# Kernel tuning notes

Measured on AMD Instinct MI355X. Metric: run time of the kernel, lower is better.

Reference implementation:

```python
import jax, jax.numpy as jnp
import numpy as np

EMBED_DIM = 1024
NUM_HEADS = 16
HEAD_DIM = EMBED_DIM // NUM_HEADS


def setup_inputs() -> dict:
    key = jax.random.key(0)
    ks = jax.random.split(key, 9)
    B, T, C = 2, 2048, EMBED_DIM
    s = 1.0 / np.sqrt(C)
    return {
        "x": jax.random.normal(ks[0], (B, T, C), dtype=jnp.float32),
        "Wq": jax.random.normal(ks[1], (C, C), dtype=jnp.float32) * s,
        "bq": jnp.zeros((C,), dtype=jnp.float32),
        "Wk": jax.random.normal(ks[2], (C, C), dtype=jnp.float32) * s,
        "bk": jnp.zeros((C,), dtype=jnp.float32),
        "Wv": jax.random.normal(ks[3], (C, C), dtype=jnp.float32) * s,
        "bv": jnp.zeros((C,), dtype=jnp.float32),
        "Wo": jax.random.normal(ks[4], (C, C), dtype=jnp.float32) * s,
        "bo": jnp.zeros((C,), dtype=jnp.float32),
    }


def reference(x, Wq, bq, Wk, bk, Wv, bv, Wo, bo):
    B, T, C = x.shape
    H, D = NUM_HEADS, HEAD_DIM
    # projections (torch Linear: x @ W.T + b; here W stored as [in,out])
    q = (x @ Wq + bq).reshape(B, T, H, D).transpose(0, 2, 1, 3)  # [B,H,T,D]
    k = (x @ Wk + bk).reshape(B, T, H, D).transpose(0, 2, 1, 3)
    v = (x @ Wv + bv).reshape(B, T, H, D).transpose(0, 2, 1, 3)
    scores = jnp.einsum("bhtd,bhsd->bhts", q, k) / jnp.sqrt(jnp.float32(D))
    causal = jnp.tril(jnp.ones((T, T), dtype=bool))  # keep lower triangle
    scores = jnp.where(causal, scores, -jnp.inf)
    weights = jax.nn.softmax(scores, axis=-1)
    attended = jnp.einsum("bhts,bhsd->bhtd", weights, v)
    attended = attended.transpose(0, 2, 1, 3).reshape(B, T, C)
    return attended @ Wo + bo
```

## Files before the change

### kernel.cpp

```cpp
#include <hip/hip_runtime.h>
#include <math.h>


#define BLOCK 256

typedef __attribute__((ext_vector_type(8))) short bf16x8;
typedef __attribute__((ext_vector_type(4))) float f32x4;
typedef __attribute__((ext_vector_type(16))) float f32x16;

__device__ inline short f2bf(float f) {
  union { float f; unsigned u; } c; c.f = f;
  unsigned u = c.u;
  unsigned r = (u + 0x7fffu + ((u >> 16) & 1u)) >> 16;
  return (short)r;
}

#define GLD_LDS16(g, l)                                            \
  __builtin_amdgcn_global_load_lds(                                \
      (const __attribute__((address_space(1))) unsigned int*)(g),  \
      (__attribute__((address_space(3))) unsigned int*)(l), 16, 0, 0)


__global__ void cvt_all_kernel(const float* __restrict__ x,
                               const float* __restrict__ Wq, const float* __restrict__ Wk,
                               const float* __restrict__ Wv, const float* __restrict__ Wo,
                               short* __restrict__ xb,
                               short* __restrict__ Wtqkv, short* __restrict__ Wto) {
  int z = blockIdx.z;
  if (z >= 4) {
    int blk = blockIdx.x + (blockIdx.y << 5) + ((z - 4) << 10);
    int i = (blk * 256 + threadIdx.x) * 8;
    float4 a = *(const float4*)(x + i);
    float4 b = *(const float4*)(x + i + 4);
    alignas(16) short o[8];
    o[0] = f2bf(a.x); o[1] = f2bf(a.y); o[2] = f2bf(a.z); o[3] = f2bf(a.w);
    o[4] = f2bf(b.x); o[5] = f2bf(b.y); o[6] = f2bf(b.z); o[7] = f2bf(b.w);
    *(int4*)(xb + i) = *(int4*)o;
    return;
  }
  __shared__ float tile[32][33];
  const float* W = (z == 0) ? Wq : (z == 1) ? Wk : (z == 2) ? Wv : Wo;
  short* outp = (z == 3) ? Wto : (Wtqkv + (size_t)z * 1024 * 1024);
  int k0 = blockIdx.x * 32, n0 = blockIdx.y * 32;
  int tr = threadIdx.x >> 5, tc = threadIdx.x & 31;
#pragma unroll
  for (int i = 0; i < 4; i++)
    tile[tr + i * 8][tc] = W[(k0 + tr + i * 8) * 1024 + n0 + tc];
  __syncthreads();
#pragma unroll
  for (int i = 0; i < 4; i++)
    outp[(n0 + tr + i * 8) * 1024 + k0 + tc] = f2bf(tile[tc][tr + i * 8]);
}


__global__ __launch_bounds__(BLOCK) void gemm_qkv_kernel(
    const short* __restrict__ A, const short* __restrict__ Wt,
    const float* __restrict__ bq, const float* __restrict__ bk,
    const float* __restrict__ bv,
    short* __restrict__ Qo, short* __restrict__ Ko, short* __restrict__ Vo) {
  const int Kd = 1024;
  const float QSCL = 0.18033688011f;
  int p = blockIdx.x;
  int xcd = p & 7, j = p >> 3;
  int m0 = ((xcd & 3) * 8 + (j & 7)) * 128;
  int n0 = ((xcd >> 2) * 12 + (j >> 3)) * 128;
  int t = threadIdx.x;
  int lane = t & 63, wv = t >> 6;
  int quad = lane >> 4, lc = lane & 15;
  int wy = wv >> 1, wx = wv & 1;
  __shared__ short As[3][128 * 32];
  __shared__ short Bs[3][128 * 32];
  f32x4 acc[4][4] = {};
  int r0 = t >> 2;
  int cs = ((t & 3) ^ ((r0 >> 1) & 3)) * 8;
  const short* Arow0 = A + (size_t)(m0 + r0) * Kd + cs;
  const short* Arow1 = A + (size_t)(m0 + r0 + 64) * Kd + cs;
  const short* Brow0 = Wt + (size_t)(n0 + r0) * Kd + cs;
  const short* Brow1 = Wt + (size_t)(n0 + r0 + 64) * Kd + cs;
#define STAGE_QKV(buf, koff)                           \
  do {                                                 \
    GLD_LDS16(Arow0 + (koff), &As[buf][8 * t]);        \
    GLD_LDS16(Arow1 + (koff), &As[buf][8 * t + 2048]); \
    GLD_LDS16(Brow0 + (koff), &Bs[buf][8 * t]);        \
    GLD_LDS16(Brow1 + (koff), &Bs[buf][8 * t + 2048]); \
  } while (0)
  STAGE_QKV(0, 0);
  asm volatile("" ::: "memory");
  STAGE_QKV(1, 32);
  int xq8 = (quad ^ ((lc >> 1) & 3)) * 8;
  int cur = 0, wr = 2;
  for (int step = 0; step < 32; step++) {
    if (step < 30)
      asm volatile("s_waitcnt vmcnt(4) lgkmcnt(0)" ::: "memory");
    else
      asm volatile("s_waitcnt vmcnt(0) lgkmcnt(0)" ::: "memory");
    __builtin_amdgcn_s_barrier();
    asm volatile("" ::: "memory");
    if (step + 2 < 32) STAGE_QKV(wr, (step + 2) * 32);
    bf16x8 af[4], bf[4];
#pragma unroll
    for (int i = 0; i < 4; i++)
      af[i] = *(const bf16x8*)&As[cur][(wy * 64 + i * 16 + lc) * 32 + xq8];
#pragma unroll
    for (int i = 0; i < 4; i++)
      bf[i] = *(const bf16x8*)&Bs[cur][(wx * 64 + i * 16 + lc) * 32 + xq8];
#pragma unroll
    for (int mi = 0; mi < 4; mi++)
#pragma unroll
      for (int ni = 0; ni < 4; ni++)
        acc[mi][ni] = __builtin_amdgcn_mfma_f32_16x16x32_bf16(af[mi], bf[ni], acc[mi][ni], 0, 0, 0);
    cur = (cur == 2) ? 0 : cur + 1;
    wr = (wr == 2) ? 0 : wr + 1;
  }
#undef STAGE_QKV
#pragma unroll
  for (int mi = 0; mi < 4; mi++) {
    int row = m0 + wy * 64 + mi * 16 + quad * 4;
#pragma unroll
    for (int ni = 0; ni < 4; ni++) {
      int col = n0 + wx * 64 + ni * 16 + lc;
      int which = col >> 10;
      int hd = col & 1023;
      int h = hd >> 6, d = hd & 63;
      float bb = (which == 0) ? bq[hd] : (which == 1) ? bk[hd] : bv[hd];
      if (which == 2) {
        alignas(8) short pk[4];
#pragma unroll
        for (int r = 0; r < 4; r++) pk[r] = f2bf(acc[mi][ni][r] + bb);
        int b = row >> 11, tt = row & 2047;
        *(int2*)&Vo[((size_t)(b * 16 + h) * 64 + d) * 2048 + tt] = *(const int2*)pk;
      } else {
#pragma unroll
        for (int r = 0; r < 4; r++) {
          int rw = row + r;
          int b = rw >> 11, tt = rw & 2047;
          float val = acc[mi][ni][r] + bb;
          if (which == 0) {
            Qo[((size_t)(b * 16 + h) * 2048 + tt) * 64 + d] = f2bf(val * QSCL);
          } else {
            Ko[((size_t)(b * 16 + h) * 2048 + tt) * 64 + d] = f2bf(val);
          }
        }
      }
    }
  }
}


__global__ __launch_bounds__(BLOCK) void gemm_out_kernel(
    const short* __restrict__ A, const short* __restrict__ Wt,
    const float* __restrict__ bias, float* __restrict__ Out) {
  const int Kd = 1024;
  int m0 = blockIdx.x * 64, n0 = blockIdx.y * 128;
  int t = threadIdx.x;
  int lane = t & 63, wv = t >> 6;
  int quad = lane >> 4, lc = lane & 15;
  int wy = wv >> 1, wx = wv & 1;
  __shared__ short As[2][64 * 32];
  __shared__ short Bs[2][128 * 32];
  int r0 = t >> 2, c0 = (t & 3) * 8;
  f32x4 acc[2][4] = {};
  const short* Arow0 = A + (size_t)(m0 + r0) * Kd + c0;
  const short* Brow0 = Wt + (size_t)(n0 + r0) * Kd + c0;
  const short* Brow1 = Wt + (size_t)(n0 + r0 + 64) * Kd + c0;
  GLD_LDS16(Arow0, &As[0][8 * t]);
  GLD_LDS16(Brow0, &Bs[0][8 * t]);
  GLD_LDS16(Brow1, &Bs[0][8 * t + 2048]);
  int cur = 0;
  for (int k0 = 0; k0 < Kd; k0 += 32) {
    __syncthreads();
    if (k0 + 32 < Kd) {
      int nxt = cur ^ 1;
      GLD_LDS16(Arow0 + k0 + 32, &As[nxt][8 * t]);
      GLD_LDS16(Brow0 + k0 + 32, &Bs[nxt][8 * t]);
      GLD_LDS16(Brow1 + k0 + 32, &Bs[nxt][8 * t + 2048]);
    }
    bf16x8 af[2], bf[4];
#pragma unroll
    for (int i = 0; i < 2; i++)
      af[i] = *(const bf16x8*)&As[cur][(wy * 32 + i * 16 + lc) * 32 + quad * 8];
#pragma unroll
    for (int i = 0; i < 4; i++)
      bf[i] = *(const bf16x8*)&Bs[cur][(wx * 64 + i * 16 + lc) * 32 + quad * 8];
#pragma unroll
    for (int mi = 0; mi < 2; mi++)
#pragma unroll
      for (int ni = 0; ni < 4; ni++)
        acc[mi][ni] = __builtin_amdgcn_mfma_f32_16x16x32_bf16(af[mi], bf[ni], acc[mi][ni], 0, 0, 0);
    cur ^= 1;
  }
#pragma unroll
  for (int mi = 0; mi < 2; mi++) {
    int row = m0 + wy * 32 + mi * 16 + quad * 4;
#pragma unroll
    for (int ni = 0; ni < 4; ni++) {
      int col = n0 + wx * 64 + ni * 16 + lc;
      float bb = bias[col];
#pragma unroll
      for (int r = 0; r < 4; r++)
        Out[(size_t)(row + r) * 1024 + col] = acc[mi][ni][r] + bb;
    }
  }
}


__global__ __launch_bounds__(BLOCK, 2) void attn_kernel(
    const short* __restrict__ Q, const short* __restrict__ K,
    const short* __restrict__ Vt, short* __restrict__ Oa) {
  int p = blockIdx.x;
  int bh = ((p & 7) << 2) | ((p >> 3) & 3);
  int pair = p >> 5;
  int t = threadIdx.x;
  int lane = t & 63, w = t >> 6;
  int qh = w & 1, kh = w >> 1;
  int ln = lane & 31, lh = lane >> 5;
  const short* Qb = Q + (size_t)bh * 2048 * 64;
  const short* Kb = K + (size_t)bh * 2048 * 64;
  const short* Vg = Vt + (size_t)bh * 64 * 2048;
  int b = bh >> 4, h = bh & 15;

  __shared__ short Kt[2][64 * 64];
  __shared__ short Vs[2][64 * 64];
  __shared__ __align__(16) short Ps[4][32 * 72];
  __shared__ float lx[2][64];
  short* Pw = Ps[w];

  int srow = t >> 3;
  int sw = t & 7;
  const float M2 = 14.5f;
  int xk = ln & 7;

  for (int sp = 0; sp < 2; sp++) {
    int s = sp ? (31 - pair) : pair;
    int q0 = s * 64;
    int q0w = q0 + qh * 32;
    int qmaxw = q0w + 31;
    int ntiles = s + 1;

    bf16x8 qf[4];
#pragma unroll
    for (int c = 0; c < 4; c++)
      qf[c] = *(const bf16x8*)&Qb[(size_t)(q0w + ln) * 64 + c * 16 + lh * 8];

    f32x16 O0 = {}, O1 = {};
    float lsum = 0.f;

#pragma unroll
    for (int i = 0; i < 2; i++) {
      int r = i * 32 + srow;
      int cg = sw ^ (r & 7);
      GLD_LDS16(&Kb[(size_t)r * 64 + cg * 8], &Kt[0][i * 2048 + 8 * t]);
      GLD_LDS16(&Vg[(size_t)r * 2048 + cg * 8], &Vs[0][i * 2048 + 8 * t]);
    }
    int cur = 0;
    for (int kt = 0; kt < ntiles; kt++) {
      __syncthreads();
      if (kt + 1 < ntiles) {
        int kb2 = (kt + 1) * 64;
        int nxt = cur ^ 1;
#pragma unroll
        for (int i = 0; i < 2; i++) {
          int r = i * 32 + srow;
          int cg = sw ^ (r & 7);
          GLD_LDS16(&Kb[(size_t)(kb2 + r) * 64 + cg * 8], &Kt[nxt][i * 2048 + 8 * t]);
          GLD_LDS16(&Vg[(size_t)r * 2048 + kb2 + cg * 8], &Vs[nxt][i * 2048 + 8 * t]);
        }
      }
      int grpbase = kt * 64 + kh * 32;
      if (grpbase <= qmaxw) {
        f32x16 S = {};
#pragma unroll
        for (int c = 0; c < 4; c++) {
          int ch = c * 2 + lh;
          bf16x8 kf = *(const bf16x8*)&Kt[cur][(kh * 32 + ln) * 64 + (ch ^ xk) * 8];
          S = __builtin_amdgcn_mfma_f32_32x32x16_bf16(kf, qf[c], S, 0, 0, 0);
        }
        if (kt == ntiles - 1) {
          int qg = q0w + ln;
#pragma unroll
          for (int reg = 0; reg < 16; reg++) {
            int key = grpbase + (reg & 3) + 8 * (reg >> 2) + 4 * lh;
            if (key > qg) S[reg] = -3.0e38f;
          }
        }
#pragma unroll
        for (int g = 0; g < 4; g++) {
          unsigned u[4];
#pragma unroll
          for (int i = 0; i < 4; i++) {
            union { float f; unsigned v; } cc;
            cc.f = __builtin_amdgcn_exp2f(S[g * 4 + i] - M2);
            lsum += cc.f;
            u[i] = cc.v + 0x8000u;
          }
          int2 pk;
          pk.x = (int)__builtin_amdgcn_perm(u[1], u[0], 0x07060302);
          pk.y = (int)__builtin_amdgcn_perm(u[3], u[2], 0x07060302);
          *(int2*)&Pw[ln * 72 + g * 8 + lh * 4] = pk;
        }
#pragma unroll
        for (int c2 = 0; c2 < 2; c2++) {
          bf16x8 pf = *(const bf16x8*)&Pw[ln * 72 + c2 * 16 + lh * 8];
          int ch = kh * 4 + c2 * 2 + lh;
          bf16x8 v0 = *(const bf16x8*)&Vs[cur][ln * 64 + (ch ^ xk) * 8];
          bf16x8 v1 = *(const bf16x8*)&Vs[cur][(32 + ln) * 64 + (ch ^ xk) * 8];
          O0 = __builtin_amdgcn_mfma_f32_32x32x16_bf16(v0, pf, O0, 0, 0, 0);
          O1 = __builtin_amdgcn_mfma_f32_32x32x16_bf16(v1, pf, O1, 0, 0, 0);
        }
      }
      cur ^= 1;
    }

    float* ob = (float*)&Ps[0][0];
    __syncthreads();
    if (kh == 1) {
      float* obw = ob + qh * 2048;
#pragma unroll
      for (int dh = 0; dh < 2; dh++)
#pragma unroll
        for (int reg = 0; reg < 16; reg++)
          obw[((dh * 16 + reg) * 2 + lh) * 32 + ln] = dh ? O1[reg] : O0[reg];
      lx[qh][lane] = lsum;
    }
    __syncthreads();
    if (kh == 0) {
      float* obw = ob + qh * 2048;
#pragma unroll
      for (int reg = 0; reg < 16; reg++) {
        O0[reg] += obw[((0 * 16 + reg) * 2 + lh) * 32 + ln];
        O1[reg] += obw[((1 * 16 + reg) * 2 + lh) * 32 + ln];
      }
      float lt = lsum + lx[qh][lane];
      lt += __shfl_xor(lt, 32, 64);
      float inv = 1.0f / lt;
      size_t rowbase = (size_t)(b * 2048 + q0w + ln) * 1024 + h * 64;
#pragma unroll
      for (int dh = 0; dh < 2; dh++)
#pragma unroll
        for (int g = 0; g < 4; g++) {
          alignas(8) short pk[4];
#pragma unroll
          for (int i = 0; i < 4; i++) {
            float v = dh ? O1[g * 4 + i] : O0[g * 4 + i];
            pk[i] = f2bf(v * inv);
          }
          *(int2*)&Oa[rowbase + dh * 32 + g * 8 + lh * 4] = *(const int2*)pk;
        }
    }
  }
}


extern "C" void kernel_launch(void* const* d_in, const int* in_sizes, int n_in,
                              void* d_out, int out_size, void* d_ws, size_t ws_size,
                              hipStream_t stream) {
  const float* x = (const float*)d_in[0];
  const float* Wq = (const float*)d_in[1];
  const float* bq = (const float*)d_in[2];
  const float* Wk = (const float*)d_in[3];
  const float* bk = (const float*)d_in[4];
  const float* Wv = (const float*)d_in[5];
  const float* bv = (const float*)d_in[6];
  const float* Wo = (const float*)d_in[7];
  const float* bo = (const float*)d_in[8];
  char* ws = (char*)d_ws;
  const size_t MB = 1024 * 1024;
  short* xb = (short*)(ws);
  short* Wtqkv = (short*)(ws + 8 * MB);
  short* Wto = (short*)(ws + 14 * MB);
  short* Qb = (short*)(ws + 17 * MB);
  short* Kb = (short*)(ws + 25 * MB);
  short* Vb = (short*)(ws + 33 * MB);
  short* Att = (short*)(ws + 41 * MB);
  float* out = (float*)d_out;

  cvt_all_kernel<<<dim3(32, 32, 6), BLOCK, 0, stream>>>(x, Wq, Wk, Wv, Wo, xb, Wtqkv, Wto);
  gemm_qkv_kernel<<<dim3(768), BLOCK, 0, stream>>>(xb, Wtqkv, bq, bk, bv, Qb, Kb, Vb);
  attn_kernel<<<512, BLOCK, 0, stream>>>(Qb, Kb, Vb, Att);
  gemm_out_kernel<<<dim3(64, 8), BLOCK, 0, stream>>>(Att, Wto, bo, out);
}
```

Before: 196.3 us.

## Restructure QKV GEMM to register-staged prefetch with single K=64 LDS tile

The QKV projection GEMM drops its triple-buffered direct global-to-LDS pipeline with K=32 tiles. It now prefetches the next K=64 slab into registers while computing on a single LDS buffer, using an XOR swizzle. This halves the number of barrier iterations and adds launch_bounds with 3 blocks per CU to target occupancy. The trade-off is two barriers per step, extra VGPRs for staging, and the loss of async LDS loads that overlapped with compute.

```diff
diff --git a/kernel.cpp b/kernel.cpp
--- a/kernel.cpp
+++ b/kernel.cpp
@@ -53,7 +53,7 @@
 }
 
 
-__global__ __launch_bounds__(BLOCK) void gemm_qkv_kernel(
+__global__ __launch_bounds__(BLOCK, 3) void gemm_qkv_kernel(
     const short* __restrict__ A, const short* __restrict__ Wt,
     const float* __restrict__ bq, const float* __restrict__ bk,
     const float* __restrict__ bv,
@@ -68,51 +68,63 @@
   int lane = t & 63, wv = t >> 6;
   int quad = lane >> 4, lc = lane & 15;
   int wy = wv >> 1, wx = wv & 1;
-  __shared__ short As[3][128 * 32];
-  __shared__ short Bs[3][128 * 32];
+  __shared__ short As[128 * 64];
+  __shared__ short Bs[128 * 64];
   f32x4 acc[4][4] = {};
-  int r0 = t >> 2;
-  int cs = ((t & 3) ^ ((r0 >> 1) & 3)) * 8;
-  const short* Arow0 = A + (size_t)(m0 + r0) * Kd + cs;
-  const short* Arow1 = A + (size_t)(m0 + r0 + 64) * Kd + cs;
-  const short* Brow0 = Wt + (size_t)(n0 + r0) * Kd + cs;
-  const short* Brow1 = Wt + (size_t)(n0 + r0 + 64) * Kd + cs;
-#define STAGE_QKV(buf, koff)                           \
-  do {                                                 \
-    GLD_LDS16(Arow0 + (koff), &As[buf][8 * t]);        \
-    GLD_LDS16(Arow1 + (koff), &As[buf][8 * t + 2048]); \
-    GLD_LDS16(Brow0 + (koff), &Bs[buf][8 * t]);        \
-    GLD_LDS16(Brow1 + (koff), &Bs[buf][8 * t + 2048]); \
-  } while (0)
-  STAGE_QKV(0, 0);
-  asm volatile("" ::: "memory");
-  STAGE_QKV(1, 32);
-  int xq8 = (quad ^ ((lc >> 1) & 3)) * 8;
-  int cur = 0, wr = 2;
-  for (int step = 0; step < 32; step++) {
-    if (step < 30)
-      asm volatile("s_waitcnt vmcnt(4) lgkmcnt(0)" ::: "memory");
-    else
-      asm volatile("s_waitcnt vmcnt(0) lgkmcnt(0)" ::: "memory");
+
+  int sr = wv * 32 + (lane >> 3);
+  int schk = lane & 7;
+  const short* Ab = A + (size_t)(m0 + sr) * Kd + schk * 8;
+  const short* Bb = Wt + (size_t)(n0 + sr) * Kd + schk * 8;
+  int wslot = schk ^ (lane >> 3);
+  short* wa = &As[sr * 64 + wslot * 8];
+  short* wb = &Bs[sr * 64 + wslot * 8];
+
+  bf16x8 sA[4], sB[4];
+#pragma unroll
+  for (int i = 0; i < 4; i++) {
+    sA[i] = *(const bf16x8*)(Ab + (size_t)(i * 8) * Kd);
+    sB[i] = *(const bf16x8*)(Bb + (size_t)(i * 8) * Kd);
+  }
+  int rx = lc & 7;
+  for (int step = 0; step < 16; step++) {
+#pragma unroll
+    for (int i = 0; i < 4; i++) {
+      *(bf16x8*)(wa + i * 8 * 64) = sA[i];
+      *(bf16x8*)(wb + i * 8 * 64) = sB[i];
+    }
+    asm volatile("s_waitcnt lgkmcnt(0)" ::: "memory");
     __builtin_amdgcn_s_barrier();
     asm volatile("" ::: "memory");
-    if (step + 2 < 32) STAGE_QKV(wr, (step + 2) * 32);
-    bf16x8 af[4], bf[4];
-#pragma unroll
-    for (int i = 0; i < 4; i++)
-      af[i] = *(const bf16x8*)&As[cur][(wy * 64 + i * 16 + lc) * 32 + xq8];
-#pragma unroll
-    for (int i = 0; i < 4; i++)
-      bf[i] = *(const bf16x8*)&Bs[cur][(wx * 64 + i * 16 + lc) * 32 + xq8];
-#pragma unroll
-    for (int mi = 0; mi < 4; mi++)
-#pragma unroll
-      for (int ni = 0; ni < 4; ni++)
-        acc[mi][ni] = __builtin_amdgcn_mfma_f32_16x16x32_bf16(af[mi], bf[ni], acc[mi][ni], 0, 0, 0);
-    cur = (cur == 2) ? 0 : cur + 1;
-    wr = (wr == 2) ? 0 : wr + 1;
-  }
-#undef STAGE_QKV
+    if (step + 1 < 16) {
+      int koff = (step + 1) * 64;
+#pragma unroll
+      for (int i = 0; i < 4; i++) {
+        sA[i] = *(const bf16x8*)(Ab + (size_t)(i * 8) * Kd + koff);
+        sB[i] = *(const bf16x8*)(Bb + (size_t)(i * 8) * Kd + koff);
+      }
+    }
+#pragma unroll
+    for (int kc = 0; kc < 2; kc++) {
+      bf16x8 af[4], bf[4];
+#pragma unroll
+      for (int i = 0; i < 4; i++)
+        af[i] = *(const bf16x8*)&As[(wy * 64 + i * 16 + lc) * 64 +
+                                    ((kc * 4 + quad) ^ rx) * 8];
+#pragma unroll
+      for (int i = 0; i < 4; i++)
+        bf[i] = *(const bf16x8*)&Bs[(wx * 64 + i * 16 + lc) * 64 +
+                                    ((kc * 4 + quad) ^ rx) * 8];
+#pragma unroll
+      for (int mi = 0; mi < 4; mi++)
+#pragma unroll
+        for (int ni = 0; ni < 4; ni++)
+          acc[mi][ni] = __builtin_amdgcn_mfma_f32_16x16x32_bf16(af[mi], bf[ni], acc[mi][ni], 0, 0, 0);
+    }
+    asm volatile("s_waitcnt lgkmcnt(0)" ::: "memory");
+    __builtin_amdgcn_s_barrier();
+    asm volatile("" ::: "memory");
+  }
 #pragma unroll
   for (int mi = 0; mi < 4; mi++) {
     int row = m0 + wy * 64 + mi * 16 + quad * 4;
```

Measured after the change: 178.3 us. 1.1x faster.
